# Optimization experiments

Measured on AMD Instinct MI355X. Metric: run time of the kernel, lower is better.

## Reference

```python
import jax, jax.numpy as jnp
import numpy as np

N_PATCH = 15  # patch_size
M_UNITS = 16  # patches_per_batch


def setup_inputs() -> dict:
    key = jax.random.key(0)
    k1, k2, k3 = jax.random.split(key, 3)
    B, C, H, W = 64, 128, 64, 64
    x = jax.random.normal(k1, (B, C, H, W), dtype=jnp.float32)
    x_cord = jax.random.randint(k2, (B, M_UNITS), 0, W)
    y_cord = jax.random.randint(k3, (B, M_UNITS), 0, H)
    return {"x": x, "x_cord": x_cord, "y_cord": y_cord}


def reference(x, x_cord, y_cord):
    # x: [B, C, H, W]; x_cord/y_cord: [B, M] integer cell indices.
    B, C, H, W = x.shape
    n = N_PATCH
    M = x_cord.shape[1]

    lin = jnp.linspace(-1.0, 1.0, n, dtype=jnp.float32)
    gy, gx = jnp.meshgrid(lin, lin, indexing="ij")  # base_grid: gx = [..,0], gy = [..,1]

    xs = x_cord.reshape(-1).astype(jnp.float32)  # [B*M]
    ys = y_cord.reshape(-1).astype(jnp.float32)
    xs_n = (xs / (W - 1) * 2.0 - 1.0)[:, None, None]
    ys_n = (ys / (H - 1) * 2.0 - 1.0)[:, None, None]
    scale_x = (n - 1) / (W - 1)
    scale_y = (n - 1) / (H - 1)

    # NOTE: the original deliberately adds ys_norm to the x-channel and xs_norm
    # to the y-channel of the grid; we replicate that exactly.
    grid_x_ch = gx * scale_x + ys_n  # grid[..., 0] -> width coord for grid_sample
    grid_y_ch = gy * scale_y + xs_n  # grid[..., 1] -> height coord

    in_bounds = ((grid_x_ch >= -1) & (grid_x_ch <= 1)
                 & (grid_y_ch >= -1) & (grid_y_ch <= 1)).astype(x.dtype)  # [B*M, n, n]

    # grid_sample(mode='nearest', align_corners=True, padding_mode='zeros')
    ix = jnp.round((grid_x_ch + 1.0) * 0.5 * (W - 1)).astype(jnp.int32)
    iy = jnp.round((grid_y_ch + 1.0) * 0.5 * (H - 1)).astype(jnp.int32)
    valid = (ix >= 0) & (ix < W) & (iy >= 0) & (iy < H)
    ixc = jnp.clip(ix, 0, W - 1)
    iyc = jnp.clip(iy, 0, H - 1)

    b_idx = jnp.repeat(jnp.arange(B), M)[:, None, None]  # [B*M,1,1]
    # Direct gather from x (no B*M expanded copy): result [B*M, n, n, C]
    patches = x[b_idx, :, iyc, ixc]
    patches = jnp.transpose(patches, (0, 3, 1, 2))  # [B*M, C, n, n]
    patches = patches * valid[:, None, :, :].astype(x.dtype)  # zero padding

    return jnp.concatenate([patches, in_bounds[:, None, :, :]], axis=1)  # [B*M, C+1, n, n]
```

## Files before the change

kernel.cpp:

```cpp
#include <hip/hip_runtime.h>


constexpr int NP    = 15;
constexpr int NPOS  = NP * NP;
constexpr int CH    = 128;
constexpr int HH    = 64, WW = 64;
constexpr int PLANE = HH * WW;
constexpr int MPB   = 16;
constexpr unsigned PER_PATCH = (CH + 1) * NPOS;

__device__ __forceinline__ float sample(const float* __restrict__ s,
                                        int xs, int ys, int pos) {
  const int i  = pos / NP;
  const int j  = pos - i * NP;
  const int ix = ys + j - 7;
  const int iy = xs + i - 7;
  if (((unsigned)ix < (unsigned)WW) && ((unsigned)iy < (unsigned)HH)) {
    const int c4 = ix >> 2, w = ix & 3;
    return s[(iy << 6) + (((c4 + iy) & 15) << 2) + w];
  }
  return 0.0f;
}

__global__ __launch_bounds__(256)
void patch_dma(const float* __restrict__ x,
               const int* __restrict__ xcord,
               const int* __restrict__ ycord,
               float* __restrict__ out) {
  const int cg = blockIdx.x;
  const int b  = blockIdx.y;
  const int t  = threadIdx.x;

  __shared__ int    sx[MPB], sy[MPB];
  __shared__ float4 s4[HH * (WW / 4)];

  if (t < MPB) { sx[t] = xcord[b * MPB + t]; sy[t] = ycord[b * MPB + t]; }

  if (cg == CH) {
    __syncthreads();
    for (int e = t; e < MPB * NPOS; e += 256) {
      const int p   = e / NPOS;
      const int pos = e - p * NPOS;
      const int i  = pos / NP;
      const int j  = pos - i * NP;
      const int xs = sx[p], ys = sy[p];
      const int ix = ys + j - 7;
      const int iy = xs + i - 7;
      const bool v = ((unsigned)ix < (unsigned)WW) && ((unsigned)iy < (unsigned)HH);
      const bool xflip = (ix == WW - 1) && (ys < WW - 1);
      const bool yflip = (iy == HH - 1) && (xs < HH - 1);
      out[(size_t)(b * MPB + p) * PER_PATCH + (size_t)CH * NPOS + pos] =
          (v && !xflip && !yflip) ? 1.0f : 0.0f;
    }
    return;
  }

  const float4* __restrict__ src =
      reinterpret_cast<const float4*>(x + ((size_t)b * CH + cg) * PLANE);
#pragma unroll
  for (int k = 0; k < 4; ++k) {
    const int slot  = k * 256 + t;
    const int row   = slot >> 4;
    const int c4p   = slot & 15;
    const int srcf4 = (row << 4) + ((c4p - row) & 15);
    float4* ldsbase = &s4[k * 256 + (t & 192)];
    __builtin_amdgcn_global_load_lds(
        (const __attribute__((address_space(1))) void*)(src + srcf4),
        (__attribute__((address_space(3))) void*)ldsbase,
        16, 0, 0);
  }
  __syncthreads();

  const float* __restrict__ s = reinterpret_cast<const float*>(s4);
  const int wv   = t >> 6;
  const int lane = t & 63;
  for (int p = wv; p < MPB; p += 4) {
    const int xs = sx[p], ys = sy[p];
    const size_t Bp = (size_t)(b * MPB + p) * PER_PATCH + (size_t)cg * NPOS;
    const int h  = (4 - (int)(Bp & 3)) & 3;
    const int nq = (NPOS - h) >> 2;
    const int r  = NPOS - h - 4 * nq;

    if (lane < h)
      out[Bp + lane] = sample(s, xs, ys, lane);

    if (lane < nq) {
      const int p0 = h + 4 * lane;
      float4 o;
      o.x = sample(s, xs, ys, p0);
      o.y = sample(s, xs, ys, p0 + 1);
      o.z = sample(s, xs, ys, p0 + 2);
      o.w = sample(s, xs, ys, p0 + 3);
      *reinterpret_cast<float4*>(out + Bp + h + 4 * (size_t)lane) = o;
    }

    if (lane < r) {
      const int pt = h + 4 * nq + lane;
      out[Bp + pt] = sample(s, xs, ys, pt);
    }
  }
}

extern "C" void kernel_launch(void* const* d_in, const int* in_sizes, int n_in,
                              void* d_out, int out_size, void* d_ws, size_t ws_size,
                              hipStream_t stream) {
  const float* x  = (const float*)d_in[0];
  const int*   xc = (const int*)d_in[1];
  const int*   yc = (const int*)d_in[2];
  float* outp = (float*)d_out;

  dim3 grid(CH + 1, 64);
  patch_dma<<<grid, 256, 0, stream>>>(x, xc, yc, outp);
}
```

Before: 44.88 us.

## Double-buffer channel planes per block with async LDS loads across 8 channels

Replaces the one-block-per-channel grid with 1024 blocks of 512 threads, each handling 8 channels of one batch. The next channel plane is staged into a second LDS buffer with global_load_lds while the current one is sampled, so load latency overlaps with sampling and stores. The separate in-bounds-mask block is folded into each block's tail, and block launch overhead is cut. The cost is fewer blocks, which gives less parallelism and occupancy from the larger LDS footprint, and manual vmcnt waits that rely on the exact number of outstanding loads.

After: 46.51 us. +3.6%, slower.

```diff
diff --git a/kernel.cpp b/kernel.cpp
--- a/kernel.cpp
+++ b/kernel.cpp
@@ -7,10 +7,14 @@
 constexpr int HH    = 64, WW = 64;
 constexpr int PLANE = HH * WW;
 constexpr int MPB   = 16;
+constexpr int TILES = 8;
 constexpr unsigned PER_PATCH = (CH + 1) * NPOS;
 
-__device__ __forceinline__ float sample(const float* __restrict__ s,
-                                        int xs, int ys, int pos) {
+typedef float f4v __attribute__((ext_vector_type(4)));
+typedef float f4a __attribute__((ext_vector_type(4), aligned(4)));
+
+__device__ __forceinline__ float sampf(const float* __restrict__ s,
+                                       int xs, int ys, int pos) {
   const int i  = pos / NP;
   const int j  = pos - i * NP;
   const int ix = ys + j - 7;
@@ -22,81 +26,94 @@
   return 0.0f;
 }
 
-__global__ __launch_bounds__(256)
-void patch_dma(const float* __restrict__ x,
-               const int* __restrict__ xcord,
-               const int* __restrict__ ycord,
-               float* __restrict__ out) {
-  const int cg = blockIdx.x;
-  const int b  = blockIdx.y;
-  const int t  = threadIdx.x;
+__global__ __launch_bounds__(512)
+void patch_pipe(const float* __restrict__ x,
+                const int* __restrict__ xcord,
+                const int* __restrict__ ycord,
+                float* __restrict__ out) {
+  const int blk = blockIdx.x;
+  const int b   = blk >> 4;
+  const int cg0 = (blk & 15) * TILES;
+  const int t   = threadIdx.x;
+  const int wv  = t >> 6, lane = t & 63;
 
-  __shared__ int    sx[MPB], sy[MPB];
-  __shared__ float4 s4[HH * (WW / 4)];
+  __shared__ int   sx[MPB], sy[MPB];
+  __shared__ float buf[2][PLANE];
 
   if (t < MPB) { sx[t] = xcord[b * MPB + t]; sy[t] = ycord[b * MPB + t]; }
+  __syncthreads();
 
-  if (cg == CH) {
-    __syncthreads();
-    for (int e = t; e < MPB * NPOS; e += 256) {
-      const int p   = e / NPOS;
-      const int pos = e - p * NPOS;
+  auto stage = [&](int k) {
+    const float4* __restrict__ src =
+        reinterpret_cast<const float4*>(x + ((size_t)b * CH + cg0 + k) * PLANE);
+    float4* dst = reinterpret_cast<float4*>(buf[k & 1]);
+#pragma unroll
+    for (int i = 0; i < 2; ++i) {
+      const int slot  = i * 512 + t;
+      const int row   = slot >> 4;
+      const int c4p   = slot & 15;
+      const int srcf4 = (row << 4) + ((c4p - row) & 15);
+      float4* ldsbase = dst + i * 512 + (t & 448);
+      __builtin_amdgcn_global_load_lds(
+          (const __attribute__((address_space(1))) void*)(src + srcf4),
+          (__attribute__((address_space(3))) void*)ldsbase,
+          16, 0, 0);
+    }
+  };
+
+  stage(0);
+  for (int k = 0; k < TILES; ++k) {
+    if (k + 1 < TILES) {
+      stage(k + 1);
+      asm volatile("s_waitcnt vmcnt(2)" ::: "memory");
+    } else {
+      asm volatile("s_waitcnt vmcnt(0)" ::: "memory");
+    }
+    __builtin_amdgcn_sched_barrier(0);
+    __builtin_amdgcn_s_barrier();
+
+    const float* __restrict__ s = buf[k & 1];
+    const int cg = cg0 + k;
+#pragma unroll
+    for (int half = 0; half < 2; ++half) {
+      const int m  = 2 * wv + half;
+      const int xs = sx[m], ys = sy[m];
+      const size_t S = (size_t)(b * MPB + m) * PER_PATCH + (size_t)cg * NPOS;
+      const int h  = (4 - (int)(S & 3)) & 3;
+      const int nq = (NPOS - h) >> 2;
+      const int rr = NPOS - h - 4 * nq;
+
+      if (lane < h) out[S + lane] = sampf(s, xs, ys, lane);
+      if (lane < nq) {
+        const int p0 = h + 4 * lane;
+        f4v o;
+        o.x = sampf(s, xs, ys, p0);
+        o.y = sampf(s, xs, ys, p0 + 1);
+        o.z = sampf(s, xs, ys, p0 + 2);
+        o.w = sampf(s, xs, ys, p0 + 3);
+        *reinterpret_cast<f4a*>(out + S + h + 4 * (size_t)lane) = o;
+      }
+      if (lane < rr) {
+        const int pt = h + 4 * nq + lane;
+        out[S + pt] = sampf(s, xs, ys, pt);
+      }
+    }
+    __builtin_amdgcn_s_barrier();
+  }
+
+  if (wv == 0) {
+    const int p  = blk;
+    const int xs = xcord[p], ys = ycord[p];
+    const size_t S = (size_t)p * PER_PATCH + (size_t)CH * NPOS;
+    for (int pos = lane; pos < NPOS; pos += 64) {
       const int i  = pos / NP;
       const int j  = pos - i * NP;
-      const int xs = sx[p], ys = sy[p];
       const int ix = ys + j - 7;
       const int iy = xs + i - 7;
-      const bool v = ((unsigned)ix < (unsigned)WW) && ((unsigned)iy < (unsigned)HH);
-      const bool xflip = (ix == WW - 1) && (ys < WW - 1);
-      const bool yflip = (iy == HH - 1) && (xs < HH - 1);
-      out[(size_t)(b * MPB + p) * PER_PATCH + (size_t)CH * NPOS + pos] =
-          (v && !xflip && !yflip) ? 1.0f : 0.0f;
-    }
-    return;
-  }
-
-  const float4* __restrict__ src =
-      reinterpret_cast<const float4*>(x + ((size_t)b * CH + cg) * PLANE);
-#pragma unroll
-  for (int k = 0; k < 4; ++k) {
-    const int slot  = k * 256 + t;
-    const int row   = slot >> 4;
-    const int c4p   = slot & 15;
-    const int srcf4 = (row << 4) + ((c4p - row) & 15);
-    float4* ldsbase = &s4[k * 256 + (t & 192)];
-    __builtin_amdgcn_global_load_lds(
-        (const __attribute__((address_space(1))) void*)(src + srcf4),
-        (__attribute__((address_space(3))) void*)ldsbase,
-        16, 0, 0);
-  }
-  __syncthreads();
-
-  const float* __restrict__ s = reinterpret_cast<const float*>(s4);
-  const int wv   = t >> 6;
-  const int lane = t & 63;
-  for (int p = wv; p < MPB; p += 4) {
-    const int xs = sx[p], ys = sy[p];
-    const size_t Bp = (size_t)(b * MPB + p) * PER_PATCH + (size_t)cg * NPOS;
-    const int h  = (4 - (int)(Bp & 3)) & 3;
-    const int nq = (NPOS - h) >> 2;
-    const int r  = NPOS - h - 4 * nq;
-
-    if (lane < h)
-      out[Bp + lane] = sample(s, xs, ys, lane);
-
-    if (lane < nq) {
-      const int p0 = h + 4 * lane;
-      float4 o;
-      o.x = sample(s, xs, ys, p0);
-      o.y = sample(s, xs, ys, p0 + 1);
-      o.z = sample(s, xs, ys, p0 + 2);
-      o.w = sample(s, xs, ys, p0 + 3);
-      *reinterpret_cast<float4*>(out + Bp + h + 4 * (size_t)lane) = o;
-    }
-
-    if (lane < r) {
-      const int pt = h + 4 * nq + lane;
-      out[Bp + pt] = sample(s, xs, ys, pt);
+      const bool v  = ((unsigned)ix < (unsigned)WW) && ((unsigned)iy < (unsigned)HH);
+      const bool xf = (ix == WW - 1) && (ys < WW - 1);
+      const bool yf = (iy == HH - 1) && (xs < HH - 1);
+      out[S + pos] = (v && !xf && !yf) ? 1.0f : 0.0f;
     }
   }
 }
@@ -109,6 +126,5 @@
   const int*   yc = (const int*)d_in[2];
   float* outp = (float*)d_out;
 
-  dim3 grid(CH + 1, 64);
-  patch_dma<<<grid, 256, 0, stream>>>(x, xc, yc, outp);
+  patch_pipe<<<1024, 512, 0, stream>>>(x, xc, yc, outp);
 }
```
